# Kernel optimization log

Hardware: AMD Instinct MI355X
Metric: run time of the kernel (lower is better)

Reference implementation:

```python
import jax, jax.numpy as jnp
import numpy as np

B, S, H, NH = 2, 2048, 1024, 16
HD = H // NH  # 64


def setup_inputs() -> dict:
    key = jax.random.key(0)
    ks = jax.random.split(key, 10)
    scale = 1.0 / np.sqrt(H)
    inp = {
        "hidden_states": jax.random.normal(ks[0], (B, S, H), dtype=jnp.float32),
        # mask: 1.0 -> masked (gets -10000 added), 0.0 -> attend
        "attention_mask": jax.random.randint(ks[1], (B, S), 0, 2).astype(jnp.float32),
        "Wq": jax.random.normal(ks[2], (H, H), dtype=jnp.float32) * scale,
        "bq": jnp.zeros((H,), dtype=jnp.float32),
        "Wk": jax.random.normal(ks[3], (H, H), dtype=jnp.float32) * scale,
        "bk": jnp.zeros((H,), dtype=jnp.float32),
        "Wv": jax.random.normal(ks[4], (H, H), dtype=jnp.float32) * scale,
        "bv": jnp.zeros((H,), dtype=jnp.float32),
        "Wo": jax.random.normal(ks[5], (H, H), dtype=jnp.float32) * scale,
        "bo": jnp.zeros((H,), dtype=jnp.float32),
    }
    return inp


def _split_heads(x):
    # [B, S, H] -> [B, NH, S, HD]
    return x.reshape(B, S, NH, HD).transpose(0, 2, 1, 3)


def reference(hidden_states, attention_mask, Wq, bq, Wk, bk, Wv, bv, Wo, bo):
    q = _split_heads(hidden_states @ Wq + bq)
    k = _split_heads(hidden_states @ Wk + bk)
    v = _split_heads(hidden_states @ Wv + bv)
    # [B, NH, S, S]
    scores = jnp.einsum("bhqd,bhkd->bhqk", q, k) / jnp.sqrt(
        jnp.asarray(HD, dtype=jnp.float32))
    # mask [B, S] -> [B, 1, 1, S]; mask==1 means masked out
    scores = scores + attention_mask[:, None, None, :] * -10000.0
    probs = jax.nn.softmax(scores, axis=-1)  # dropout = identity (eval)
    ctx = jnp.einsum("bhqk,bhkd->bhqd", probs, v)
    ctx = ctx.transpose(0, 2, 1, 3).reshape(B, S, H)
    return ctx @ Wo + bo
```

## Files before the change

### kernel.cpp

```cpp
#include <hip/hip_runtime.h>
#include <hip/hip_bf16.h>
#include <math.h>

#define NB 2
#define SS 2048
#define HH 1024
#define NHEAD 16
#define HDIM 64
#define NTOK (NB * SS)

#define QSCALE 0.18033688011112042f

typedef __attribute__((ext_vector_type(8))) short short8;
typedef __attribute__((ext_vector_type(4))) float f32x4;
typedef __attribute__((ext_vector_type(16))) float f32x16;

#define SWZ16(row, boff) ((boff) ^ (((row) & 7) << 4))

__device__ __forceinline__ unsigned short f2b(float x) {
    union { float f; unsigned int u; } v; v.f = x;
    unsigned int u = v.u + 0x7fff + ((v.u >> 16) & 1);
    return (unsigned short)(u >> 16);
}

__device__ __forceinline__ unsigned pk2a(float lo, float hi) {
    unsigned r;
    asm("v_cvt_pk_bf16_f32 %0, %1, %2" : "=v"(r) : "v"(lo), "v"(hi));
    return r;
}

__device__ __forceinline__ float exp2fast(float x) {
#if __has_builtin(__builtin_amdgcn_exp2f)
    return __builtin_amdgcn_exp2f(x);
#else
    return exp2f(x);
#endif
}

__device__ __forceinline__ void gl16(const void* g, void* l) {
    __builtin_amdgcn_global_load_lds(
        (const __attribute__((address_space(1))) void*)g,
        (__attribute__((address_space(3))) void*)l, 16, 0, 0);
}

__global__ __launch_bounds__(256) void prep(
    const float* __restrict__ hs,
    const float* __restrict__ mask,
    const float* __restrict__ W0, const float* __restrict__ W1,
    const float* __restrict__ W2, const float* __restrict__ W3,
    unsigned short* __restrict__ Ab,
    unsigned short* __restrict__ Wt,
    int* __restrict__ idx, float* __restrict__ bias, int* __restrict__ cnt)
{
    __shared__ unsigned short T[64][72];
    __shared__ int part[256];
    const int bid = blockIdx.x;
    const int tid = threadIdx.x;

    if (bid < 2048) {
        const size_t i = ((size_t)bid * 256 + tid) * 8;
        float4 v0 = *(const float4*)(hs + i);
        float4 v1 = *(const float4*)(hs + i + 4);
        short8 o;
        o[0] = f2b(v0.x); o[1] = f2b(v0.y); o[2] = f2b(v0.z); o[3] = f2b(v0.w);
        o[4] = f2b(v1.x); o[5] = f2b(v1.y); o[6] = f2b(v1.z); o[7] = f2b(v1.w);
        *(short8*)(Ab + i) = o;
    } else if (bid < 3072) {
        const int t = bid - 2048;
        const int z = t >> 8;
        const int n0 = (t & 15) * 64, k0 = ((t >> 4) & 15) * 64;
        const float* W = z == 0 ? W0 : z == 1 ? W1 : z == 2 ? W2 : W3;
        unsigned short* dst = Wt + (size_t)z * HH * HH;
        {
            const int r = tid >> 2, c4 = (tid & 3) * 16;
            const float* src = W + (size_t)(k0 + r) * HH + n0 + c4;
#pragma unroll
            for (int j = 0; j < 16; j += 4) {
                float4 v = *(const float4*)(src + j);
                T[c4 + j + 0][r] = f2b(v.x); T[c4 + j + 1][r] = f2b(v.y);
                T[c4 + j + 2][r] = f2b(v.z); T[c4 + j + 3][r] = f2b(v.w);
            }
        }
        __syncthreads();
        {
            const int n = tid >> 2, sc = (tid & 3) * 2;
#pragma unroll
            for (int u = 0; u < 2; ++u) {
                short8 v = *(const short8*)&T[n][(sc + u) * 8];
                *(short8*)(dst + (size_t)(n0 + n) * HH + k0 + (sc + u) * 8) = v;
            }
        }
    } else {
        const int b = bid - 3072;
        int loc[8]; int m = 0;
        const float* mp = mask + (size_t)b * SS + tid * 8;
#pragma unroll
        for (int j = 0; j < 8; ++j) { loc[j] = (mp[j] == 0.0f) ? 1 : 0; m += loc[j]; }
        part[tid] = m;
        __syncthreads();
        for (int d = 1; d < 256; d <<= 1) {
            int v = (tid >= d) ? part[tid - d] : 0;
            __syncthreads();
            part[tid] += v;
            __syncthreads();
        }
        int base = part[tid] - m;
        const int total = part[255];
#pragma unroll
        for (int j = 0; j < 8; ++j)
            if (loc[j]) idx[(size_t)b * SS + (base++)] = tid * 8 + j;
        if (tid == 0) cnt[b] = total;
        __syncthreads();
        for (int j = tid; j < SS; j += 256) {
            if (j >= total) idx[(size_t)b * SS + j] = 0;
            bias[(size_t)b * SS + j] = (j < total) ? 0.0f : -1e30f;
        }
    }
}

__global__ __launch_bounds__(256) void gemm_qkv(
    const unsigned short* __restrict__ A, const unsigned short* __restrict__ Bt,
    const float* __restrict__ b0, const float* __restrict__ b1,
    const float* __restrict__ b2, unsigned short* __restrict__ Cout)
{
    __shared__ __align__(16) unsigned short As[2][128 * 32];
    __shared__ __align__(16) unsigned short Bs[2][128 * 32];

    const int tid = threadIdx.x;
    const int w  = tid >> 6;
    const int l  = tid & 63;
    const int g  = l >> 4, c = l & 15;
    const int wr = w >> 1, wc = w & 1;
    const int m0 = blockIdx.y * 128, n0 = blockIdx.x * 128;

    const int srow = l >> 2;
    const int gch  = (l & 3) ^ (srow & 3);

    f32x4 acc[4][4];
#pragma unroll
    for (int mi = 0; mi < 4; ++mi)
#pragma unroll
        for (int ni = 0; ni < 4; ++ni)
            acc[mi][ni] = (f32x4){0.f, 0.f, 0.f, 0.f};

#define STAGE(kt_, bb) {                                                      \
    _Pragma("unroll")                                                         \
    for (int u_ = 0; u_ < 2; ++u_) {                                          \
        const int rb_ = (w * 2 + u_) * 16;                                    \
        gl16(A  + (size_t)(m0 + rb_ + srow) * HH + (kt_) * 32 + gch * 8,      \
             (void*)&As[bb][rb_ * 32]);                                       \
        gl16(Bt + (size_t)(n0 + rb_ + srow) * HH + (kt_) * 32 + gch * 8,      \
             (void*)&Bs[bb][rb_ * 32]);                                       \
    } }

    STAGE(0, 0);
    STAGE(1, 1);

    for (int kt = 0; kt < 32; ++kt) {
        const int cb = kt & 1;
        if (kt < 31) asm volatile("s_waitcnt vmcnt(4)" ::: "memory");
        else         asm volatile("s_waitcnt vmcnt(0)" ::: "memory");
        __builtin_amdgcn_s_barrier();
        __builtin_amdgcn_sched_barrier(0);

        short8 af[4], bf[4];
#pragma unroll
        for (int mi = 0; mi < 4; ++mi) {
            const int row = wr * 64 + mi * 16 + c;
            af[mi] = *(const short8*)&As[cb][row * 32 + ((g * 8) ^ ((c & 3) * 8))];
        }
#pragma unroll
        for (int ni = 0; ni < 4; ++ni) {
            const int row = wc * 64 + ni * 16 + c;
            bf[ni] = *(const short8*)&Bs[cb][row * 32 + ((g * 8) ^ ((c & 3) * 8))];
        }
        __builtin_amdgcn_s_setprio(1);
#pragma unroll
        for (int mi = 0; mi < 4; ++mi)
#pragma unroll
            for (int ni = 0; ni < 4; ++ni)
                acc[mi][ni] = __builtin_amdgcn_mfma_f32_16x16x32_bf16(
                    af[mi], bf[ni], acc[mi][ni], 0, 0, 0);
        __builtin_amdgcn_s_setprio(0);

        __builtin_amdgcn_sched_barrier(0);
        __builtin_amdgcn_s_barrier();
        __builtin_amdgcn_sched_barrier(0);
        if (kt + 2 < 32) STAGE(kt + 2, cb);
    }
#undef STAGE

    const int which = n0 >> 10;
    const float* bp = which == 0 ? b0 : which == 1 ? b1 : b2;
    const float scl = which == 0 ? QSCALE : 1.0f;
    unsigned short* dst = Cout + (size_t)which * NTOK * HH;
#pragma unroll
    for (int ni = 0; ni < 4; ++ni) {
        const int nl = (n0 + wc * 64 + ni * 16 + c) & 1023;
        const int h = nl >> 6, d = nl & 63;
        const float bv = bp[nl];
#pragma unroll
        for (int mi = 0; mi < 4; ++mi) {
            const int mBase = m0 + wr * 64 + mi * 16 + g * 4;
#pragma unroll
            for (int j = 0; j < 4; ++j) {
                const int m = mBase + j;
                const int b = m >> 11, si = m & 2047;
                dst[(((size_t)(b * 16 + h)) * SS + si) * 64 + d] =
                    f2b((acc[mi][ni][j] + bv) * scl);
            }
        }
    }
}

__global__ __launch_bounds__(256) void gemm_out(
    const unsigned short* __restrict__ A, const unsigned short* __restrict__ Bt,
    const float* __restrict__ b0, float* __restrict__ Cout)
{
    __shared__ __align__(16) unsigned short As[2][128 * 64];
    __shared__ __align__(16) unsigned short Bs[2][128 * 64];

    const int tid = threadIdx.x;
    const int w  = tid >> 6;
    const int l  = tid & 63;
    const int g  = l >> 4, c = l & 15;
    const int wr = w >> 1, wc = w & 1;
    const int m0 = blockIdx.y * 128, n0 = blockIdx.x * 128;

    const int dr = l >> 3;
    const int gc = (l & 7) ^ dr;

    const unsigned short* aBase = A  + (size_t)(m0 + w * 32 + dr) * HH + gc * 8;
    const unsigned short* bBase = Bt + (size_t)(n0 + w * 32 + dr) * HH + gc * 8;

    f32x4 acc[4][4];
#pragma unroll
    for (int mi = 0; mi < 4; ++mi)
#pragma unroll
        for (int ni = 0; ni < 4; ++ni)
            acc[mi][ni] = (f32x4){0.f, 0.f, 0.f, 0.f};

    const int swz = (c & 7) * 8;

#define STAGE(kt_, bb) {                                                      \
    const int koff = (kt_) * 64;                                              \
    _Pragma("unroll")                                                         \
    for (int i_ = 0; i_ < 4; ++i_) {                                          \
        gl16(aBase + koff + (size_t)i_ * 8 * HH, (void*)&As[bb][(w*4+i_)*512]); \
        gl16(bBase + koff + (size_t)i_ * 8 * HH, (void*)&Bs[bb][(w*4+i_)*512]); \
    } }

    STAGE(0, 0);
    STAGE(1, 1);

    for (int kt = 0; kt < 16; ++kt) {
        const int cb = kt & 1;
        if (kt < 15) asm volatile("s_waitcnt vmcnt(8)" ::: "memory");
        else         asm volatile("s_waitcnt vmcnt(0)" ::: "memory");
        __builtin_amdgcn_s_barrier();
        __builtin_amdgcn_sched_barrier(0);

        short8 af[2][4], bf[2][4];
#pragma unroll
        for (int ks = 0; ks < 2; ++ks) {
            const int kb = ks * 32;
#pragma unroll
            for (int mi = 0; mi < 4; ++mi) {
                const int row = wr * 64 + mi * 16 + c;
                af[ks][mi] = *(const short8*)&As[cb][row * 64 + ((kb + g * 8) ^ swz)];
            }
#pragma unroll
            for (int ni = 0; ni < 4; ++ni) {
                const int row = wc * 64 + ni * 16 + c;
                bf[ks][ni] = *(const short8*)&Bs[cb][row * 64 + ((kb + g * 8) ^ swz)];
            }
        }
        __builtin_amdgcn_s_setprio(1);
#pragma unroll
        for (int ks = 0; ks < 2; ++ks)
#pragma unroll
            for (int mi = 0; mi < 4; ++mi)
#pragma unroll
                for (int ni = 0; ni < 4; ++ni)
                    acc[mi][ni] = __builtin_amdgcn_mfma_f32_16x16x32_bf16(
                        af[ks][mi], bf[ks][ni], acc[mi][ni], 0, 0, 0);
        __builtin_amdgcn_s_setprio(0);

        __builtin_amdgcn_sched_barrier(0);
        __builtin_amdgcn_s_barrier();
        __builtin_amdgcn_sched_barrier(0);
        if (kt + 2 < 16) STAGE(kt + 2, cb);
    }
#undef STAGE

#pragma unroll
    for (int ni = 0; ni < 4; ++ni) {
        const int n = n0 + wc * 64 + ni * 16 + c;
        const float bv = b0[n];
#pragma unroll
        for (int mi = 0; mi < 4; ++mi) {
            const int mBase = m0 + wr * 64 + mi * 16 + g * 4;
#pragma unroll
            for (int j = 0; j < 4; ++j)
                Cout[(size_t)(mBase + j) * HH + n] = acc[mi][ni][j] + bv;
        }
    }
}

__global__ __launch_bounds__(256) void vtrans(
    const unsigned short* __restrict__ Vh, const int* __restrict__ idx,
    unsigned short* __restrict__ Vt)
{
    __shared__ unsigned short T[64][72];
    const int tid = threadIdx.x;
    const int bh = blockIdx.y;
    const int b  = bh >> 4;
    const int s0 = blockIdx.x * 64;
    {
        const int r = tid >> 2, dc = (tid & 3) * 16;
        const int sidx = idx[(size_t)b * SS + s0 + r];
        const unsigned short* src = Vh + ((size_t)bh * SS + sidx) * 64 + dc;
        short8 v0 = *(const short8*)src;
        short8 v1 = *(const short8*)(src + 8);
#pragma unroll
        for (int j = 0; j < 8; ++j) {
            T[dc + j][r]     = (unsigned short)v0[j];
            T[dc + 8 + j][r] = (unsigned short)v1[j];
        }
    }
    __syncthreads();
    {
        const int d = tid >> 2, sc = (tid & 3) * 2;
#pragma unroll
        for (int u = 0; u < 2; ++u) {
            short8 v = *(const short8*)&T[d][(sc + u) * 8];
            *(short8*)(Vt + ((size_t)bh * 64 + d) * SS + s0 + (sc + u) * 8) = v;
        }
    }
}

__global__ __launch_bounds__(256) void attn_mfma(
    const unsigned short* __restrict__ Qb, const unsigned short* __restrict__ Kb,
    const unsigned short* __restrict__ Vtb, const float* __restrict__ biasg,
    const int* __restrict__ idxg, const int* __restrict__ cntg,
    unsigned short* __restrict__ ctx)
{
    __shared__ __align__(16) unsigned short Ks[2][64 * 64];
    __shared__ __align__(16) unsigned short Vts[2][64 * 64];
    __shared__ float Sc[4][32];

    const int wg  = blockIdx.x;
    const int swg = (wg & 7) * 64 + (wg >> 3);
    const int qx  = swg & 15;
    const int bh  = swg >> 4;

    const int tid = threadIdx.x;
    const int l   = tid & 63;
    const int wq  = tid >> 6;
    const int hi  = l >> 5;
    const int c   = l & 31;
    const int b   = bh >> 4, h = bh & 15;
    const int q0  = qx * 128 + wq * 32;

    const unsigned short* Qp = Qb  + (size_t)bh * SS * 64;
    const unsigned short* Kp = Kb  + (size_t)bh * SS * 64;
    const unsigned short* Vp = Vtb + (size_t)bh * 64 * SS;
    const float* biasp = biasg + (size_t)b * SS;
    const int* idxb = idxg + (size_t)b * SS;

    const int cnt    = cntg[b];
    const int nt     = (cnt + 63) >> 6;
    const int ntFull = cnt >> 6;

    const int sr  = tid >> 3;
    const int sc8 = tid & 7;

    short8 qf[4];
    {
        const unsigned short* qrow = Qp + (size_t)(q0 + c) * 64 + hi * 8;
#pragma unroll
        for (int s = 0; s < 4; ++s) qf[s] = *(const short8*)(qrow + s * 16);
    }

    f32x16 oacc[2];
#pragma unroll
    for (int dt = 0; dt < 2; ++dt)
#pragma unroll
        for (int r = 0; r < 16; ++r) oacc[dt][r] = 0.f;

    float ls[4] = {0.f, 0.f, 0.f, 0.f};

    short8 kr0, kr1, vr0, vr1;

#define LOADREG(t_) {                                                         \
    const int* ip_ = idxb + (t_) * 64;                                        \
    const int sA_ = ip_[sr], sB_ = ip_[sr + 32];                              \
    kr0 = *(const short8*)(Kp + (size_t)sA_ * 64 + sc8 * 8);                  \
    kr1 = *(const short8*)(Kp + (size_t)sB_ * 64 + sc8 * 8);                  \
    vr0 = *(const short8*)(Vp + (size_t)sr * SS + (t_) * 64 + sc8 * 8);       \
    vr1 = *(const short8*)(Vp + (size_t)(sr + 32) * SS + (t_) * 64 + sc8 * 8); }

#define DSWRITE(bb) {                                                         \
    *(short8*)((char*)Ks[bb]  + sr * 128        + SWZ16(sr, sc8 * 16)) = kr0; \
    *(short8*)((char*)Ks[bb]  + (sr + 32) * 128 + SWZ16(sr + 32, sc8 * 16)) = kr1; \
    *(short8*)((char*)Vts[bb] + sr * 128        + SWZ16(sr, sc8 * 16)) = vr0; \
    *(short8*)((char*)Vts[bb] + (sr + 32) * 128 + SWZ16(sr + 32, sc8 * 16)) = vr1; }

    LOADREG(0);
    DSWRITE(0);
    __syncthreads();

    for (int t = 0; t < nt; ++t) {
        const int cb = t & 1;
        if (t + 1 < nt) LOADREG(t + 1);
        const bool needBias = (t >= ntFull);

#pragma unroll
        for (int hh = 0; hh < 2; ++hh) {
            f32x16 s4h;
#pragma unroll
            for (int r = 0; r < 16; ++r) s4h[r] = 0.f;
            const int krow = hh * 32 + c;
            __builtin_amdgcn_s_setprio(1);
#pragma unroll
            for (int ss = 0; ss < 4; ++ss) {
                short8 kf = *(const short8*)((char*)Ks[cb] + krow * 128 +
                                             SWZ16(krow, (ss * 2 + hi) * 16));
                s4h = __builtin_amdgcn_mfma_f32_32x32x16_bf16(kf, qf[ss], s4h, 0, 0, 0);
            }
            __builtin_amdgcn_s_setprio(0);

            float pvv[16];
            if (needBias) {
                f32x4 mqh[4];
#pragma unroll
                for (int tt = 0; tt < 4; ++tt)
                    mqh[tt] = *(const f32x4*)(biasp + t * 64 + (hh * 4 + tt) * 8 + hi * 4);
#pragma unroll
                for (int r = 0; r < 16; ++r)
                    pvv[r] = exp2fast(s4h[r] + mqh[r >> 2][r & 3]);
            } else {
#pragma unroll
                for (int r = 0; r < 16; ++r)
                    pvv[r] = exp2fast(s4h[r]);
            }
#pragma unroll
            for (int r = 0; r < 16; ++r) ls[r & 3] += pvv[r];

            unsigned wdh[8];
#pragma unroll
            for (int j = 0; j < 8; ++j) wdh[j] = pk2a(pvv[2 * j], pvv[2 * j + 1]);
#pragma unroll
            for (int g4 = 0; g4 < 2; ++g4) {
                asm volatile("v_permlane32_swap_b32 %0, %1"
                             : "+v"(wdh[4 * g4 + 0]), "+v"(wdh[4 * g4 + 2]));
                asm volatile("v_permlane32_swap_b32 %0, %1"
                             : "+v"(wdh[4 * g4 + 1]), "+v"(wdh[4 * g4 + 3]));
            }

            __builtin_amdgcn_s_setprio(1);
#pragma unroll
            for (int s2 = 0; s2 < 2; ++s2) {
                const int ss = hh * 2 + s2;
                union { unsigned u[4]; short8 s8; } pa;
#pragma unroll
                for (int u_ = 0; u_ < 4; ++u_) pa.u[u_] = wdh[4 * s2 + u_];
#pragma unroll
                for (int dt = 0; dt < 2; ++dt) {
                    const int vrow = dt * 32 + c;
                    short8 vf = *(const short8*)((char*)Vts[cb] + vrow * 128 +
                                                 SWZ16(vrow, (ss * 2 + hi) * 16));
                    oacc[dt] = __builtin_amdgcn_mfma_f32_32x32x16_bf16(pa.s8, vf, oacc[dt], 0, 0, 0);
                }
            }
            __builtin_amdgcn_s_setprio(0);
        }

        if (t + 1 < nt) DSWRITE(cb ^ 1);
        __syncthreads();
    }
#undef LOADREG
#undef DSWRITE

    float lsum = (ls[0] + ls[1]) + (ls[2] + ls[3]);
    lsum += __shfl_xor(lsum, 32, 64);

    Sc[wq][c] = lsum;
    asm volatile("s_waitcnt lgkmcnt(0)" ::: "memory");
    f32x4 lq[4];
#pragma unroll
    for (int tt = 0; tt < 4; ++tt)
        lq[tt] = *(const f32x4*)&Sc[wq][tt * 8 + hi * 4];

#pragma unroll
    for (int dt = 0; dt < 2; ++dt)
#pragma unroll
        for (int r = 0; r < 16; ++r) {
            const int row = (r & 3) + 8 * (r >> 2) + 4 * hi;
            const float val = oacc[dt][r] / lq[r >> 2][r & 3];
            ctx[((size_t)(b * SS + q0 + row)) * HH + h * 64 + dt * 32 + c] = f2b(val);
        }
}

extern "C" void kernel_launch(void* const* d_in, const int* in_sizes, int n_in,
                              void* d_out, int out_size, void* d_ws, size_t ws_size,
                              hipStream_t stream)
{
    const float* hs   = (const float*)d_in[0];
    const float* mask = (const float*)d_in[1];
    const float* Wq   = (const float*)d_in[2];
    const float* bq   = (const float*)d_in[3];
    const float* Wk   = (const float*)d_in[4];
    const float* bk   = (const float*)d_in[5];
    const float* Wv   = (const float*)d_in[6];
    const float* bv   = (const float*)d_in[7];
    const float* Wo   = (const float*)d_in[8];
    const float* bo   = (const float*)d_in[9];
    float* out = (float*)d_out;

    unsigned short* Ab   = (unsigned short*)d_ws;
    unsigned short* Wt   = Ab + (size_t)NTOK * HH;
    unsigned short* Qh   = Wt + (size_t)4 * HH * HH;
    unsigned short* Kh   = Qh + (size_t)NTOK * HH;
    unsigned short* Vh   = Kh + (size_t)NTOK * HH;
    unsigned short* Vt   = Vh + (size_t)NTOK * HH;
    unsigned short* ctxb = Vt + (size_t)NTOK * HH;
    float* biasb = (float*)(ctxb + (size_t)NTOK * HH);
    int*   idxb  = (int*)(biasb + (size_t)NB * SS);
    int*   cntb  = idxb + (size_t)NB * SS;

    dim3 blk(256);

    prep<<<dim3(3074), blk, 0, stream>>>(hs, mask, Wq, Wk, Wv, Wo,
                                         Ab, Wt, idxb, biasb, cntb);

    gemm_qkv<<<dim3(24, 32), blk, 0, stream>>>(Ab, Wt, bq, bk, bv, Qh);

    vtrans<<<dim3(SS / 64, NB * NHEAD), blk, 0, stream>>>(Vh, idxb, Vt);

    attn_mfma<<<dim3(512), blk, 0, stream>>>(Qh, Kh, Vt, biasb, idxb, cntb, ctxb);

    gemm_out<<<dim3(8, 32), blk, 0, stream>>>(ctxb, Wt + 3 * (size_t)HH * HH,
                                              bo, out);
}
```

Baseline: 101.6 us.

## Split attention key range across waves and halve output GEMM tile width

The attention kernel now assigns 32 query rows per workgroup, with the four waves each taking a quarter of a 128-key tile. Partial outputs and row sums are reduced through shared memory at the end, which quadruples the grid to 2048 blocks. K/V staging loses its double buffering and adds an extra barrier per tile. The output GEMM uses 128x64 tiles to double its block count, trading per-block data reuse for occupancy on the many-CU device.

```diff
diff --git a/kernel.cpp b/kernel.cpp
--- a/kernel.cpp
+++ b/kernel.cpp
@@ -16,6 +16,7 @@
 typedef __attribute__((ext_vector_type(16))) float f32x16;
 
 #define SWZ16(row, boff) ((boff) ^ (((row) & 7) << 4))
+#define VSWZ(row, boff)  ((boff) ^ (((row) & 15) << 4))
 
 __device__ __forceinline__ unsigned short f2b(float x) {
     union { float f; unsigned int u; } v; v.f = x;
@@ -218,26 +219,25 @@
     const float* __restrict__ b0, float* __restrict__ Cout)
 {
     __shared__ __align__(16) unsigned short As[2][128 * 64];
-    __shared__ __align__(16) unsigned short Bs[2][128 * 64];
+    __shared__ __align__(16) unsigned short Bs[2][64 * 64];
 
     const int tid = threadIdx.x;
     const int w  = tid >> 6;
     const int l  = tid & 63;
     const int g  = l >> 4, c = l & 15;
     const int wr = w >> 1, wc = w & 1;
-    const int m0 = blockIdx.y * 128, n0 = blockIdx.x * 128;
+    const int m0 = blockIdx.y * 128, n0 = blockIdx.x * 64;
 
     const int dr = l >> 3;
     const int gc = (l & 7) ^ dr;
 
     const unsigned short* aBase = A  + (size_t)(m0 + w * 32 + dr) * HH + gc * 8;
-    const unsigned short* bBase = Bt + (size_t)(n0 + w * 32 + dr) * HH + gc * 8;
-
-    f32x4 acc[4][4];
+
+    f32x4 acc[4][2];
 #pragma unroll
     for (int mi = 0; mi < 4; ++mi)
 #pragma unroll
-        for (int ni = 0; ni < 4; ++ni)
+        for (int ni = 0; ni < 2; ++ni)
             acc[mi][ni] = (f32x4){0.f, 0.f, 0.f, 0.f};
 
     const int swz = (c & 7) * 8;
@@ -245,9 +245,13 @@
 #define STAGE(kt_, bb) {                                                      \
     const int koff = (kt_) * 64;                                              \
     _Pragma("unroll")                                                         \
-    for (int i_ = 0; i_ < 4; ++i_) {                                          \
+    for (int i_ = 0; i_ < 4; ++i_)                                            \
         gl16(aBase + koff + (size_t)i_ * 8 * HH, (void*)&As[bb][(w*4+i_)*512]); \
-        gl16(bBase + koff + (size_t)i_ * 8 * HH, (void*)&Bs[bb][(w*4+i_)*512]); \
+    _Pragma("unroll")                                                         \
+    for (int u_ = 0; u_ < 2; ++u_) {                                          \
+        const int rb_ = (w * 2 + u_) * 8;                                     \
+        gl16(Bt + (size_t)(n0 + rb_ + dr) * HH + koff + gc * 8,               \
+             (void*)&Bs[bb][rb_ * 64]);                                       \
     } }
 
     STAGE(0, 0);
@@ -255,12 +259,12 @@
 
     for (int kt = 0; kt < 16; ++kt) {
         const int cb = kt & 1;
-        if (kt < 15) asm volatile("s_waitcnt vmcnt(8)" ::: "memory");
+        if (kt < 15) asm volatile("s_waitcnt vmcnt(6)" ::: "memory");
         else         asm volatile("s_waitcnt vmcnt(0)" ::: "memory");
         __builtin_amdgcn_s_barrier();
         __builtin_amdgcn_sched_barrier(0);
 
-        short8 af[2][4], bf[2][4];
+        short8 af[2][4], bf[2][2];
 #pragma unroll
         for (int ks = 0; ks < 2; ++ks) {
             const int kb = ks * 32;
@@ -270,8 +274,8 @@
                 af[ks][mi] = *(const short8*)&As[cb][row * 64 + ((kb + g * 8) ^ swz)];
             }
 #pragma unroll
-            for (int ni = 0; ni < 4; ++ni) {
-                const int row = wc * 64 + ni * 16 + c;
+            for (int ni = 0; ni < 2; ++ni) {
+                const int row = wc * 32 + ni * 16 + c;
                 bf[ks][ni] = *(const short8*)&Bs[cb][row * 64 + ((kb + g * 8) ^ swz)];
             }
         }
@@ -281,7 +285,7 @@
 #pragma unroll
             for (int mi = 0; mi < 4; ++mi)
 #pragma unroll
-                for (int ni = 0; ni < 4; ++ni)
+                for (int ni = 0; ni < 2; ++ni)
                     acc[mi][ni] = __builtin_amdgcn_mfma_f32_16x16x32_bf16(
                         af[ks][mi], bf[ks][ni], acc[mi][ni], 0, 0, 0);
         __builtin_amdgcn_s_setprio(0);
@@ -294,8 +298,8 @@
 #undef STAGE
 
 #pragma unroll
-    for (int ni = 0; ni < 4; ++ni) {
-        const int n = n0 + wc * 64 + ni * 16 + c;
+    for (int ni = 0; ni < 2; ++ni) {
+        const int n = n0 + wc * 32 + ni * 16 + c;
         const float bv = b0[n];
 #pragma unroll
         for (int mi = 0; mi < 4; ++mi) {
@@ -345,14 +349,14 @@
     const int* __restrict__ idxg, const int* __restrict__ cntg,
     unsigned short* __restrict__ ctx)
 {
-    __shared__ __align__(16) unsigned short Ks[2][64 * 64];
-    __shared__ __align__(16) unsigned short Vts[2][64 * 64];
-    __shared__ float Sc[4][32];
+    __shared__ __align__(16) unsigned short Ks[128 * 64];
+    __shared__ __align__(16) unsigned short Vts[64 * 128];
+    __shared__ float Lp[4][32];
 
     const int wg  = blockIdx.x;
-    const int swg = (wg & 7) * 64 + (wg >> 3);
-    const int qx  = swg & 15;
-    const int bh  = swg >> 4;
+    const int swg = (wg & 7) * 256 + (wg >> 3);
+    const int qx  = swg & 63;
+    const int bh  = swg >> 6;
 
     const int tid = threadIdx.x;
     const int l   = tid & 63;
@@ -360,7 +364,7 @@
     const int hi  = l >> 5;
     const int c   = l & 31;
     const int b   = bh >> 4, h = bh & 15;
-    const int q0  = qx * 128 + wq * 32;
+    const int q0  = qx * 32;
 
     const unsigned short* Qp = Qb  + (size_t)bh * SS * 64;
     const unsigned short* Kp = Kb  + (size_t)bh * SS * 64;
@@ -369,11 +373,13 @@
     const int* idxb = idxg + (size_t)b * SS;
 
     const int cnt    = cntg[b];
-    const int nt     = (cnt + 63) >> 6;
-    const int ntFull = cnt >> 6;
-
-    const int sr  = tid >> 3;
-    const int sc8 = tid & 7;
+    const int nt     = (cnt + 127) >> 7;
+    const int ntFull = cnt >> 7;
+
+    const int krow0 = tid >> 3;
+    const int sc8   = tid & 7;
+    const int vd    = tid >> 2;
+    const int vc0   = (tid & 3) * 4;
 
     short8 qf[4];
     {
@@ -390,94 +396,101 @@
 
     float ls[4] = {0.f, 0.f, 0.f, 0.f};
 
-    short8 kr0, kr1, vr0, vr1;
+    short8 kr0, kr1, kr2, kr3, vr0, vr1, vr2, vr3;
 
 #define LOADREG(t_) {                                                         \
-    const int* ip_ = idxb + (t_) * 64;                                        \
-    const int sA_ = ip_[sr], sB_ = ip_[sr + 32];                              \
-    kr0 = *(const short8*)(Kp + (size_t)sA_ * 64 + sc8 * 8);                  \
-    kr1 = *(const short8*)(Kp + (size_t)sB_ * 64 + sc8 * 8);                  \
-    vr0 = *(const short8*)(Vp + (size_t)sr * SS + (t_) * 64 + sc8 * 8);       \
-    vr1 = *(const short8*)(Vp + (size_t)(sr + 32) * SS + (t_) * 64 + sc8 * 8); }
-
-#define DSWRITE(bb) {                                                         \
-    *(short8*)((char*)Ks[bb]  + sr * 128        + SWZ16(sr, sc8 * 16)) = kr0; \
-    *(short8*)((char*)Ks[bb]  + (sr + 32) * 128 + SWZ16(sr + 32, sc8 * 16)) = kr1; \
-    *(short8*)((char*)Vts[bb] + sr * 128        + SWZ16(sr, sc8 * 16)) = vr0; \
-    *(short8*)((char*)Vts[bb] + (sr + 32) * 128 + SWZ16(sr + 32, sc8 * 16)) = vr1; }
+    const int* ip_ = idxb + (t_) * 128;                                       \
+    kr0 = *(const short8*)(Kp + (size_t)ip_[krow0      ] * 64 + sc8 * 8);     \
+    kr1 = *(const short8*)(Kp + (size_t)ip_[krow0 + 32 ] * 64 + sc8 * 8);     \
+    kr2 = *(const short8*)(Kp + (size_t)ip_[krow0 + 64 ] * 64 + sc8 * 8);     \
+    kr3 = *(const short8*)(Kp + (size_t)ip_[krow0 + 96 ] * 64 + sc8 * 8);     \
+    const unsigned short* vp_ = Vp + (size_t)vd * SS + (t_) * 128;            \
+    vr0 = *(const short8*)(vp_ + (vc0 + 0) * 8);                              \
+    vr1 = *(const short8*)(vp_ + (vc0 + 1) * 8);                              \
+    vr2 = *(const short8*)(vp_ + (vc0 + 2) * 8);                              \
+    vr3 = *(const short8*)(vp_ + (vc0 + 3) * 8); }
+
+#define DSWRITE() {                                                           \
+    *(short8*)((char*)Ks + (krow0      ) * 128 + SWZ16(krow0,      sc8 * 16)) = kr0; \
+    *(short8*)((char*)Ks + (krow0 + 32 ) * 128 + SWZ16(krow0 + 32, sc8 * 16)) = kr1; \
+    *(short8*)((char*)Ks + (krow0 + 64 ) * 128 + SWZ16(krow0 + 64, sc8 * 16)) = kr2; \
+    *(short8*)((char*)Ks + (krow0 + 96 ) * 128 + SWZ16(krow0 + 96, sc8 * 16)) = kr3; \
+    *(short8*)((char*)Vts + vd * 256 + VSWZ(vd, (vc0 + 0) * 16)) = vr0;       \
+    *(short8*)((char*)Vts + vd * 256 + VSWZ(vd, (vc0 + 1) * 16)) = vr1;       \
+    *(short8*)((char*)Vts + vd * 256 + VSWZ(vd, (vc0 + 2) * 16)) = vr2;       \
+    *(short8*)((char*)Vts + vd * 256 + VSWZ(vd, (vc0 + 3) * 16)) = vr3; }
 
     LOADREG(0);
-    DSWRITE(0);
+    DSWRITE();
     __syncthreads();
 
     for (int t = 0; t < nt; ++t) {
-        const int cb = t & 1;
         if (t + 1 < nt) LOADREG(t + 1);
         const bool needBias = (t >= ntFull);
 
-#pragma unroll
-        for (int hh = 0; hh < 2; ++hh) {
-            f32x16 s4h;
-#pragma unroll
-            for (int r = 0; r < 16; ++r) s4h[r] = 0.f;
-            const int krow = hh * 32 + c;
-            __builtin_amdgcn_s_setprio(1);
-#pragma unroll
-            for (int ss = 0; ss < 4; ++ss) {
-                short8 kf = *(const short8*)((char*)Ks[cb] + krow * 128 +
-                                             SWZ16(krow, (ss * 2 + hi) * 16));
-                s4h = __builtin_amdgcn_mfma_f32_32x32x16_bf16(kf, qf[ss], s4h, 0, 0, 0);
+        f32x16 s4h;
+#pragma unroll
+        for (int r = 0; r < 16; ++r) s4h[r] = 0.f;
+        const int krow = wq * 32 + c;
+        __builtin_amdgcn_s_setprio(1);
+#pragma unroll
+        for (int dd = 0; dd < 4; ++dd) {
+            short8 kf = *(const short8*)((char*)Ks + krow * 128 +
+                                         SWZ16(krow, (dd * 2 + hi) * 16));
+            s4h = __builtin_amdgcn_mfma_f32_32x32x16_bf16(kf, qf[dd], s4h, 0, 0, 0);
+        }
+        __builtin_amdgcn_s_setprio(0);
+
+        float pvv[16];
+        if (needBias) {
+            f32x4 mqh[4];
+#pragma unroll
+            for (int tt = 0; tt < 4; ++tt)
+                mqh[tt] = *(const f32x4*)(biasp + t * 128 + wq * 32 + tt * 8 + hi * 4);
+#pragma unroll
+            for (int r = 0; r < 16; ++r)
+                pvv[r] = exp2fast(s4h[r] + mqh[r >> 2][r & 3]);
+        } else {
+#pragma unroll
+            for (int r = 0; r < 16; ++r)
+                pvv[r] = exp2fast(s4h[r]);
+        }
+#pragma unroll
+        for (int r = 0; r < 16; ++r) ls[r & 3] += pvv[r];
+
+        unsigned wdh[8];
+#pragma unroll
+        for (int j = 0; j < 8; ++j) wdh[j] = pk2a(pvv[2 * j], pvv[2 * j + 1]);
+#pragma unroll
+        for (int g4 = 0; g4 < 2; ++g4) {
+            asm volatile("v_permlane32_swap_b32 %0, %1"
+                         : "+v"(wdh[4 * g4 + 0]), "+v"(wdh[4 * g4 + 2]));
+            asm volatile("v_permlane32_swap_b32 %0, %1"
+                         : "+v"(wdh[4 * g4 + 1]), "+v"(wdh[4 * g4 + 3]));
+        }
+
+        __builtin_amdgcn_s_setprio(1);
+#pragma unroll
+        for (int s2 = 0; s2 < 2; ++s2) {
+            union { unsigned u[4]; short8 s8; } pa;
+#pragma unroll
+            for (int u_ = 0; u_ < 4; ++u_) pa.u[u_] = wdh[4 * s2 + u_];
+#pragma unroll
+            for (int dt = 0; dt < 2; ++dt) {
+                const int vrow = dt * 32 + c;
+                const int vchunk = wq * 4 + s2 * 2 + hi;
+                short8 vf = *(const short8*)((char*)Vts + vrow * 256 +
+                                             VSWZ(vrow, vchunk * 16));
+                oacc[dt] = __builtin_amdgcn_mfma_f32_32x32x16_bf16(pa.s8, vf, oacc[dt], 0, 0, 0);
             }
-            __builtin_amdgcn_s_setprio(0);
-
-            float pvv[16];
-            if (needBias) {
-                f32x4 mqh[4];
-#pragma unroll
-                for (int tt = 0; tt < 4; ++tt)
-                    mqh[tt] = *(const f32x4*)(biasp + t * 64 + (hh * 4 + tt) * 8 + hi * 4);
-#pragma unroll
-                for (int r = 0; r < 16; ++r)
-                    pvv[r] = exp2fast(s4h[r] + mqh[r >> 2][r & 3]);
-            } else {
-#pragma unroll
-                for (int r = 0; r < 16; ++r)
-                    pvv[r] = exp2fast(s4h[r]);
-            }
-#pragma unroll
-            for (int r = 0; r < 16; ++r) ls[r & 3] += pvv[r];
-
-            unsigned wdh[8];
-#pragma unroll
-            for (int j = 0; j < 8; ++j) wdh[j] = pk2a(pvv[2 * j], pvv[2 * j + 1]);
-#pragma unroll
-            for (int g4 = 0; g4 < 2; ++g4) {
-                asm volatile("v_permlane32_swap_b32 %0, %1"
-                             : "+v"(wdh[4 * g4 + 0]), "+v"(wdh[4 * g4 + 2]));
-                asm volatile("v_permlane32_swap_b32 %0, %1"
-                             : "+v"(wdh[4 * g4 + 1]), "+v"(wdh[4 * g4 + 3]));
-            }
-
-            __builtin_amdgcn_s_setprio(1);
-#pragma unroll
-            for (int s2 = 0; s2 < 2; ++s2) {
-                const int ss = hh * 2 + s2;
-                union { unsigned u[4]; short8 s8; } pa;
-#pragma unroll
-                for (int u_ = 0; u_ < 4; ++u_) pa.u[u_] = wdh[4 * s2 + u_];
-#pragma unroll
-                for (int dt = 0; dt < 2; ++dt) {
-                    const int vrow = dt * 32 + c;
-                    short8 vf = *(const short8*)((char*)Vts[cb] + vrow * 128 +
-                                                 SWZ16(vrow, (ss * 2 + hi) * 16));
-                    oacc[dt] = __builtin_amdgcn_mfma_f32_32x32x16_bf16(pa.s8, vf, oacc[dt], 0, 0, 0);
-                }
-            }
-            __builtin_amdgcn_s_setprio(0);
-        }
-
-        if (t + 1 < nt) DSWRITE(cb ^ 1);
+        }
+        __builtin_amdgcn_s_setprio(0);
+
         __syncthreads();
+        if (t + 1 < nt) {
+            DSWRITE();
+            __syncthreads();
+        }
     }
 #undef LOADREG
 #undef DSWRITE
@@ -485,21 +498,39 @@
     float lsum = (ls[0] + ls[1]) + (ls[2] + ls[3]);
     lsum += __shfl_xor(lsum, 32, 64);
 
-    Sc[wq][c] = lsum;
-    asm volatile("s_waitcnt lgkmcnt(0)" ::: "memory");
-    f32x4 lq[4];
-#pragma unroll
-    for (int tt = 0; tt < 4; ++tt)
-        lq[tt] = *(const f32x4*)&Sc[wq][tt * 8 + hi * 4];
-
+    float* Ow = ((wq < 2) ? (float*)Ks : (float*)Vts) + (size_t)(wq & 1) * 2048;
 #pragma unroll
     for (int dt = 0; dt < 2; ++dt)
 #pragma unroll
         for (int r = 0; r < 16; ++r) {
-            const int row = (r & 3) + 8 * (r >> 2) + 4 * hi;
-            const float val = oacc[dt][r] / lq[r >> 2][r & 3];
-            ctx[((size_t)(b * SS + q0 + row)) * HH + h * 64 + dt * 32 + c] = f2b(val);
-        }
+            const int qrow = (r & 3) + 8 * (r >> 2) + 4 * hi;
+            Ow[qrow * 64 + dt * 32 + c] = oacc[dt][r];
+        }
+    if (hi == 0) Lp[wq][c] = lsum;
+    __syncthreads();
+
+    {
+        const int q  = tid >> 3;
+        const int d0 = (tid & 7) * 8;
+        const int o  = q * 64 + d0;
+        const float* R0 = (const float*)Ks;
+        const float* R1 = (const float*)Ks + 2048;
+        const float* R2 = (const float*)Vts;
+        const float* R3 = (const float*)Vts + 2048;
+        f32x4 s0 = *(const f32x4*)(R0 + o);
+        f32x4 s1 = *(const f32x4*)(R0 + o + 4);
+        s0 += *(const f32x4*)(R1 + o);     s1 += *(const f32x4*)(R1 + o + 4);
+        s0 += *(const f32x4*)(R2 + o);     s1 += *(const f32x4*)(R2 + o + 4);
+        s0 += *(const f32x4*)(R3 + o);     s1 += *(const f32x4*)(R3 + o + 4);
+        const float lq = (Lp[0][q] + Lp[1][q]) + (Lp[2][q] + Lp[3][q]);
+        const float inv = 1.0f / lq;
+        short8 o8;
+#pragma unroll
+        for (int j = 0; j < 4; ++j) o8[j]     = (short)f2b(s0[j] * inv);
+#pragma unroll
+        for (int j = 0; j < 4; ++j) o8[4 + j] = (short)f2b(s1[j] * inv);
+        *(short8*)(ctx + ((size_t)(b * SS + q0 + q)) * HH + h * 64 + d0) = o8;
+    }
 }
 
 extern "C" void kernel_launch(void* const* d_in, const int* in_sizes, int n_in,
@@ -538,8 +569,8 @@
 
     vtrans<<<dim3(SS / 64, NB * NHEAD), blk, 0, stream>>>(Vh, idxb, Vt);
 
-    attn_mfma<<<dim3(512), blk, 0, stream>>>(Qh, Kh, Vt, biasb, idxb, cntb, ctxb);
-
-    gemm_out<<<dim3(8, 32), blk, 0, stream>>>(ctxb, Wt + 3 * (size_t)HH * HH,
-                                              bo, out);
-}
+    attn_mfma<<<dim3(2048), blk, 0, stream>>>(Qh, Kh, Vt, biasb, idxb, cntb, ctxb);
+
+    gemm_out<<<dim3(16, 32), blk, 0, stream>>>(ctxb, Wt + 3 * (size_t)HH * HH,
+                                               bo, out);
+}
```

Measured after the change: 115.8 us. +14.0%, slower.

## Process two query tiles per attention wave and narrow output GEMM tile

Applied to the files above, without the earlier changes.

Each attention wave now handles 64 query rows (two 32-row sub-tiles) instead of 32. Each K fragment read from shared memory feeds two MFMAs, which halves K/V staging per query and halves the grid to 256 blocks. Separately, the output projection GEMM tile is narrowed from 128 to 64 columns, doubling its grid to 512 blocks for better CU fill. The cost is higher register pressure in attention and fewer attention workgroups on a 256-CU device, which may hurt occupancy.

```diff
diff --git a/kernel.cpp b/kernel.cpp
--- a/kernel.cpp
+++ b/kernel.cpp
@@ -218,26 +218,25 @@
     const float* __restrict__ b0, float* __restrict__ Cout)
 {
     __shared__ __align__(16) unsigned short As[2][128 * 64];
-    __shared__ __align__(16) unsigned short Bs[2][128 * 64];
+    __shared__ __align__(16) unsigned short Bs[2][64 * 64];
 
     const int tid = threadIdx.x;
     const int w  = tid >> 6;
     const int l  = tid & 63;
     const int g  = l >> 4, c = l & 15;
     const int wr = w >> 1, wc = w & 1;
-    const int m0 = blockIdx.y * 128, n0 = blockIdx.x * 128;
+    const int m0 = blockIdx.y * 128, n0 = blockIdx.x * 64;
 
     const int dr = l >> 3;
     const int gc = (l & 7) ^ dr;
 
     const unsigned short* aBase = A  + (size_t)(m0 + w * 32 + dr) * HH + gc * 8;
-    const unsigned short* bBase = Bt + (size_t)(n0 + w * 32 + dr) * HH + gc * 8;
-
-    f32x4 acc[4][4];
+
+    f32x4 acc[4][2];
 #pragma unroll
     for (int mi = 0; mi < 4; ++mi)
 #pragma unroll
-        for (int ni = 0; ni < 4; ++ni)
+        for (int ni = 0; ni < 2; ++ni)
             acc[mi][ni] = (f32x4){0.f, 0.f, 0.f, 0.f};
 
     const int swz = (c & 7) * 8;
@@ -245,9 +244,13 @@
 #define STAGE(kt_, bb) {                                                      \
     const int koff = (kt_) * 64;                                              \
     _Pragma("unroll")                                                         \
-    for (int i_ = 0; i_ < 4; ++i_) {                                          \
+    for (int i_ = 0; i_ < 4; ++i_)                                            \
         gl16(aBase + koff + (size_t)i_ * 8 * HH, (void*)&As[bb][(w*4+i_)*512]); \
-        gl16(bBase + koff + (size_t)i_ * 8 * HH, (void*)&Bs[bb][(w*4+i_)*512]); \
+    _Pragma("unroll")                                                         \
+    for (int u_ = 0; u_ < 2; ++u_) {                                          \
+        const int rb_ = (w * 2 + u_) * 8;                                     \
+        gl16(Bt + (size_t)(n0 + rb_ + dr) * HH + koff + gc * 8,               \
+             (void*)&Bs[bb][rb_ * 64]);                                       \
     } }
 
     STAGE(0, 0);
@@ -255,12 +258,12 @@
 
     for (int kt = 0; kt < 16; ++kt) {
         const int cb = kt & 1;
-        if (kt < 15) asm volatile("s_waitcnt vmcnt(8)" ::: "memory");
+        if (kt < 15) asm volatile("s_waitcnt vmcnt(6)" ::: "memory");
         else         asm volatile("s_waitcnt vmcnt(0)" ::: "memory");
         __builtin_amdgcn_s_barrier();
         __builtin_amdgcn_sched_barrier(0);
 
-        short8 af[2][4], bf[2][4];
+        short8 af[2][4], bf[2][2];
 #pragma unroll
         for (int ks = 0; ks < 2; ++ks) {
             const int kb = ks * 32;
@@ -270,8 +273,8 @@
                 af[ks][mi] = *(const short8*)&As[cb][row * 64 + ((kb + g * 8) ^ swz)];
             }
 #pragma unroll
-            for (int ni = 0; ni < 4; ++ni) {
-                const int row = wc * 64 + ni * 16 + c;
+            for (int ni = 0; ni < 2; ++ni) {
+                const int row = wc * 32 + ni * 16 + c;
                 bf[ks][ni] = *(const short8*)&Bs[cb][row * 64 + ((kb + g * 8) ^ swz)];
             }
         }
@@ -281,7 +284,7 @@
 #pragma unroll
             for (int mi = 0; mi < 4; ++mi)
 #pragma unroll
-                for (int ni = 0; ni < 4; ++ni)
+                for (int ni = 0; ni < 2; ++ni)
                     acc[mi][ni] = __builtin_amdgcn_mfma_f32_16x16x32_bf16(
                         af[ks][mi], bf[ks][ni], acc[mi][ni], 0, 0, 0);
         __builtin_amdgcn_s_setprio(0);
@@ -294,8 +297,8 @@
 #undef STAGE
 
 #pragma unroll
-    for (int ni = 0; ni < 4; ++ni) {
-        const int n = n0 + wc * 64 + ni * 16 + c;
+    for (int ni = 0; ni < 2; ++ni) {
+        const int n = n0 + wc * 32 + ni * 16 + c;
         const float bv = b0[n];
 #pragma unroll
         for (int mi = 0; mi < 4; ++mi) {
@@ -347,12 +350,12 @@
 {
     __shared__ __align__(16) unsigned short Ks[2][64 * 64];
     __shared__ __align__(16) unsigned short Vts[2][64 * 64];
-    __shared__ float Sc[4][32];
+    __shared__ float Sc[4][64];
 
     const int wg  = blockIdx.x;
-    const int swg = (wg & 7) * 64 + (wg >> 3);
-    const int qx  = swg & 15;
-    const int bh  = swg >> 4;
+    const int swg = (wg & 7) * 32 + (wg >> 3);
+    const int qx  = swg & 7;
+    const int bh  = swg >> 3;
 
     const int tid = threadIdx.x;
     const int l   = tid & 63;
@@ -360,7 +363,7 @@
     const int hi  = l >> 5;
     const int c   = l & 31;
     const int b   = bh >> 4, h = bh & 15;
-    const int q0  = qx * 128 + wq * 32;
+    const int q0  = qx * 256 + wq * 64;
 
     const unsigned short* Qp = Qb  + (size_t)bh * SS * 64;
     const unsigned short* Kp = Kb  + (size_t)bh * SS * 64;
@@ -375,20 +378,26 @@
     const int sr  = tid >> 3;
     const int sc8 = tid & 7;
 
-    short8 qf[4];
+    short8 qfA[4], qfB[4];
     {
-        const unsigned short* qrow = Qp + (size_t)(q0 + c) * 64 + hi * 8;
-#pragma unroll
-        for (int s = 0; s < 4; ++s) qf[s] = *(const short8*)(qrow + s * 16);
-    }
-
-    f32x16 oacc[2];
-#pragma unroll
-    for (int dt = 0; dt < 2; ++dt)
-#pragma unroll
-        for (int r = 0; r < 16; ++r) oacc[dt][r] = 0.f;
-
-    float ls[4] = {0.f, 0.f, 0.f, 0.f};
+        const unsigned short* qrA = Qp + (size_t)(q0 + c) * 64 + hi * 8;
+        const unsigned short* qrB = Qp + (size_t)(q0 + 32 + c) * 64 + hi * 8;
+#pragma unroll
+        for (int s = 0; s < 4; ++s) {
+            qfA[s] = *(const short8*)(qrA + s * 16);
+            qfB[s] = *(const short8*)(qrB + s * 16);
+        }
+    }
+
+    f32x16 oaccA[2], oaccB[2];
+#pragma unroll
+    for (int dt = 0; dt < 2; ++dt) {
+#pragma unroll
+        for (int r = 0; r < 16; ++r) { oaccA[dt][r] = 0.f; oaccB[dt][r] = 0.f; }
+    }
+
+    float lsA[4] = {0.f, 0.f, 0.f, 0.f};
+    float lsB[4] = {0.f, 0.f, 0.f, 0.f};
 
     short8 kr0, kr1, vr0, vr1;
 
@@ -417,60 +426,83 @@
 
 #pragma unroll
         for (int hh = 0; hh < 2; ++hh) {
-            f32x16 s4h;
-#pragma unroll
-            for (int r = 0; r < 16; ++r) s4h[r] = 0.f;
+            short8 kf[4];
             const int krow = hh * 32 + c;
+#pragma unroll
+            for (int dd = 0; dd < 4; ++dd)
+                kf[dd] = *(const short8*)((char*)Ks[cb] + krow * 128 +
+                                          SWZ16(krow, (dd * 2 + hi) * 16));
+
+            f32x16 s4A, s4B;
+#pragma unroll
+            for (int r = 0; r < 16; ++r) { s4A[r] = 0.f; s4B[r] = 0.f; }
             __builtin_amdgcn_s_setprio(1);
 #pragma unroll
-            for (int ss = 0; ss < 4; ++ss) {
-                short8 kf = *(const short8*)((char*)Ks[cb] + krow * 128 +
-                                             SWZ16(krow, (ss * 2 + hi) * 16));
-                s4h = __builtin_amdgcn_mfma_f32_32x32x16_bf16(kf, qf[ss], s4h, 0, 0, 0);
+            for (int dd = 0; dd < 4; ++dd) {
+                s4A = __builtin_amdgcn_mfma_f32_32x32x16_bf16(kf[dd], qfA[dd], s4A, 0, 0, 0);
+                s4B = __builtin_amdgcn_mfma_f32_32x32x16_bf16(kf[dd], qfB[dd], s4B, 0, 0, 0);
             }
             __builtin_amdgcn_s_setprio(0);
 
-            float pvv[16];
+            float pvA[16], pvB[16];
             if (needBias) {
                 f32x4 mqh[4];
 #pragma unroll
                 for (int tt = 0; tt < 4; ++tt)
                     mqh[tt] = *(const f32x4*)(biasp + t * 64 + (hh * 4 + tt) * 8 + hi * 4);
 #pragma unroll
-                for (int r = 0; r < 16; ++r)
-                    pvv[r] = exp2fast(s4h[r] + mqh[r >> 2][r & 3]);
+                for (int r = 0; r < 16; ++r) {
+                    pvA[r] = exp2fast(s4A[r] + mqh[r >> 2][r & 3]);
+                    pvB[r] = exp2fast(s4B[r] + mqh[r >> 2][r & 3]);
+                }
             } else {
 #pragma unroll
-                for (int r = 0; r < 16; ++r)
-                    pvv[r] = exp2fast(s4h[r]);
-            }
-#pragma unroll
-            for (int r = 0; r < 16; ++r) ls[r & 3] += pvv[r];
-
-            unsigned wdh[8];
-#pragma unroll
-            for (int j = 0; j < 8; ++j) wdh[j] = pk2a(pvv[2 * j], pvv[2 * j + 1]);
+                for (int r = 0; r < 16; ++r) {
+                    pvA[r] = exp2fast(s4A[r]);
+                    pvB[r] = exp2fast(s4B[r]);
+                }
+            }
+#pragma unroll
+            for (int r = 0; r < 16; ++r) {
+                lsA[r & 3] += pvA[r];
+                lsB[r & 3] += pvB[r];
+            }
+
+            unsigned wdA[8], wdB[8];
+#pragma unroll
+            for (int j = 0; j < 8; ++j) {
+                wdA[j] = pk2a(pvA[2 * j], pvA[2 * j + 1]);
+                wdB[j] = pk2a(pvB[2 * j], pvB[2 * j + 1]);
+            }
 #pragma unroll
             for (int g4 = 0; g4 < 2; ++g4) {
                 asm volatile("v_permlane32_swap_b32 %0, %1"
-                             : "+v"(wdh[4 * g4 + 0]), "+v"(wdh[4 * g4 + 2]));
+                             : "+v"(wdA[4 * g4 + 0]), "+v"(wdA[4 * g4 + 2]));
                 asm volatile("v_permlane32_swap_b32 %0, %1"
-                             : "+v"(wdh[4 * g4 + 1]), "+v"(wdh[4 * g4 + 3]));
+                             : "+v"(wdA[4 * g4 + 1]), "+v"(wdA[4 * g4 + 3]));
+                asm volatile("v_permlane32_swap_b32 %0, %1"
+                             : "+v"(wdB[4 * g4 + 0]), "+v"(wdB[4 * g4 + 2]));
+                asm volatile("v_permlane32_swap_b32 %0, %1"
+                             : "+v"(wdB[4 * g4 + 1]), "+v"(wdB[4 * g4 + 3]));
             }
 
             __builtin_amdgcn_s_setprio(1);
 #pragma unroll
             for (int s2 = 0; s2 < 2; ++s2) {
                 const int ss = hh * 2 + s2;
-                union { unsigned u[4]; short8 s8; } pa;
-#pragma unroll
-                for (int u_ = 0; u_ < 4; ++u_) pa.u[u_] = wdh[4 * s2 + u_];
+                union { unsigned u[4]; short8 s8; } paA, paB;
+#pragma unroll
+                for (int u_ = 0; u_ < 4; ++u_) {
+                    paA.u[u_] = wdA[4 * s2 + u_];
+                    paB.u[u_] = wdB[4 * s2 + u_];
+                }
 #pragma unroll
                 for (int dt = 0; dt < 2; ++dt) {
                     const int vrow = dt * 32 + c;
                     short8 vf = *(const short8*)((char*)Vts[cb] + vrow * 128 +
                                                  SWZ16(vrow, (ss * 2 + hi) * 16));
-                    oacc[dt] = __builtin_amdgcn_mfma_f32_32x32x16_bf16(pa.s8, vf, oacc[dt], 0, 0, 0);
+                    oaccA[dt] = __builtin_amdgcn_mfma_f32_32x32x16_bf16(paA.s8, vf, oaccA[dt], 0, 0, 0);
+                    oaccB[dt] = __builtin_amdgcn_mfma_f32_32x32x16_bf16(paB.s8, vf, oaccB[dt], 0, 0, 0);
                 }
             }
             __builtin_amdgcn_s_setprio(0);
@@ -482,23 +514,30 @@
 #undef LOADREG
 #undef DSWRITE
 
-    float lsum = (ls[0] + ls[1]) + (ls[2] + ls[3]);
-    lsum += __shfl_xor(lsum, 32, 64);
-
-    Sc[wq][c] = lsum;
+    float lsumA = (lsA[0] + lsA[1]) + (lsA[2] + lsA[3]);
+    float lsumB = (lsB[0] + lsB[1]) + (lsB[2] + lsB[3]);
+    lsumA += __shfl_xor(lsumA, 32, 64);
+    lsumB += __shfl_xor(lsumB, 32, 64);
+
+    Sc[wq][c]      = lsumA;
+    Sc[wq][32 + c] = lsumB;
     asm volatile("s_waitcnt lgkmcnt(0)" ::: "memory");
-    f32x4 lq[4];
-#pragma unroll
-    for (int tt = 0; tt < 4; ++tt)
-        lq[tt] = *(const f32x4*)&Sc[wq][tt * 8 + hi * 4];
+    f32x4 lqA[4], lqB[4];
+#pragma unroll
+    for (int tt = 0; tt < 4; ++tt) {
+        lqA[tt] = *(const f32x4*)&Sc[wq][tt * 8 + hi * 4];
+        lqB[tt] = *(const f32x4*)&Sc[wq][32 + tt * 8 + hi * 4];
+    }
 
 #pragma unroll
     for (int dt = 0; dt < 2; ++dt)
 #pragma unroll
         for (int r = 0; r < 16; ++r) {
             const int row = (r & 3) + 8 * (r >> 2) + 4 * hi;
-            const float val = oacc[dt][r] / lq[r >> 2][r & 3];
-            ctx[((size_t)(b * SS + q0 + row)) * HH + h * 64 + dt * 32 + c] = f2b(val);
+            const float vA = oaccA[dt][r] / lqA[r >> 2][r & 3];
+            const float vB = oaccB[dt][r] / lqB[r >> 2][r & 3];
+            ctx[((size_t)(b * SS + q0 + row)) * HH + h * 64 + dt * 32 + c] = f2b(vA);
+            ctx[((size_t)(b * SS + q0 + 32 + row)) * HH + h * 64 + dt * 32 + c] = f2b(vB);
         }
 }
 
@@ -538,8 +577,8 @@
 
     vtrans<<<dim3(SS / 64, NB * NHEAD), blk, 0, stream>>>(Vh, idxb, Vt);
 
-    attn_mfma<<<dim3(512), blk, 0, stream>>>(Qh, Kh, Vt, biasb, idxb, cntb, ctxb);
-
-    gemm_out<<<dim3(8, 32), blk, 0, stream>>>(ctxb, Wt + 3 * (size_t)HH * HH,
-                                              bo, out);
-}
+    attn_mfma<<<dim3(256), blk, 0, stream>>>(Qh, Kh, Vt, biasb, idxb, cntb, ctxb);
+
+    gemm_out<<<dim3(16, 32), blk, 0, stream>>>(ctxb, Wt + 3 * (size_t)HH * HH,
+                                               bo, out);
+}
```

Measured after the change: 108.5 us. 1.07x slower.
